# Kernel optimization log

Hardware: AMD Instinct MI355X
Metric: run time of the kernel (lower is better)

The kernel has to match this reference:

```python
import jax, jax.numpy as jnp
import numpy as np

N, S, D_MODEL, H = 8, 1024, 1024, 16
D = D_MODEL // H
NEG = -1e9


def setup_inputs() -> dict:
    key = jax.random.key(0)
    ks = jax.random.split(key, 12)
    s = 0.02
    q = jax.random.normal(ks[0], (N, S, D_MODEL), jnp.float32)
    k = jax.random.normal(ks[1], (N, S, D_MODEL), jnp.float32)
    v = jax.random.normal(ks[2], (N, S, D_MODEL), jnp.float32)
    # causal mask: 1 where masked (strict upper triangle)
    causal_mask = jnp.triu(jnp.ones((S, S), jnp.int32), k=1)
    # padding mask: 1 where key position is padding
    padding_mask = jax.random.randint(ks[3], (N, S), 0, 2, jnp.int32)
    Wq = jax.random.normal(ks[4], (D_MODEL, D_MODEL), jnp.float32) * s
    bq = jnp.zeros((D_MODEL,), jnp.float32)
    Wk = jax.random.normal(ks[5], (D_MODEL, D_MODEL), jnp.float32) * s
    bk = jnp.zeros((D_MODEL,), jnp.float32)
    Wv = jax.random.normal(ks[6], (D_MODEL, D_MODEL), jnp.float32) * s
    bv = jnp.zeros((D_MODEL,), jnp.float32)
    Wo = jax.random.normal(ks[7], (D_MODEL, D_MODEL), jnp.float32) * s
    bo = jnp.zeros((D_MODEL,), jnp.float32)
    return {"q": q, "k": k, "v": v, "causal_mask": causal_mask,
            "padding_mask": padding_mask, "Wq": Wq, "bq": bq, "Wk": Wk,
            "bk": bk, "Wv": Wv, "bv": bv, "Wo": Wo, "bo": bo}


def reference(q, k, v, causal_mask, padding_mask, Wq, bq, Wk, bk, Wv, bv, Wo, bo):
    n, qs, _ = q.shape
    # projections (nn.Linear: x @ W.T + b)
    qp = (q @ Wq.T + bq).reshape(n, qs, H, D).transpose(0, 2, 1, 3)  # [N,H,qS,D]
    kp = (k @ Wk.T + bk).reshape(n, -1, H, D).transpose(0, 2, 1, 3)  # [N,H,kS,D]
    vp = (v @ Wv.T + bv).reshape(n, -1, H, D).transpose(0, 2, 1, 3)  # [N,H,kS,D]
    # NOTE: faithful to source -- scale by sqrt(d_model), not sqrt(d_head)
    score = jnp.einsum('bhqd,bhkd->bhqk', qp, kp) / jnp.sqrt(jnp.float32(D_MODEL))
    score = jnp.where(causal_mask[None, None, :, :] == 1, NEG, score)
    score = jnp.where(padding_mask[:, None, None, :] == 1, NEG, score)
    w = jax.nn.softmax(score, axis=-1)  # dropout is identity in eval mode
    x = jnp.einsum('bhqk,bhkd->bhqd', w, vp)  # [N,H,qS,D]
    x = x.transpose(0, 2, 1, 3).reshape(n, qs, D_MODEL)
    x = x @ Wo.T + bo
    return (x, w)
```

## Files before the change

kernel.cpp:

```cpp
#include <hip/hip_runtime.h>

typedef __bf16 bf16;
typedef bf16 bf16x8 __attribute__((ext_vector_type(8)));
typedef bf16 bf16x4 __attribute__((ext_vector_type(4)));
typedef float f32x4 __attribute__((ext_vector_type(4)));

#define S_LEN 1024
#define DM    1024
#define NH    16
#define HD    64
#define NB    8
#define NEGV  (-1e9f)

#define EPI_HEADS 0
#define EPI_VT    1
#define EPI_OUT   2

__device__ __forceinline__ void async16(const bf16* g, const bf16* l) {
    __builtin_amdgcn_global_load_lds(
        (const __attribute__((address_space(1))) void*)g,
        (__attribute__((address_space(3))) void*)l, 16, 0, 0);
}

__global__ __launch_bounds__(256) void cast_all(
    const float* __restrict__ q, const float* __restrict__ k,
    const float* __restrict__ v, const float* __restrict__ wq,
    const float* __restrict__ wk, const float* __restrict__ wv,
    const float* __restrict__ wo, bf16* __restrict__ out)
{
    size_t idx = ((size_t)blockIdx.x * 256 + threadIdx.x) * 4;
    const float* src;
    size_t soff;
    if (idx < 25165824) {
        int seg = (int)(idx >> 23);
        soff = idx & 8388607;
        src = seg == 0 ? q : (seg == 1 ? k : v);
    } else {
        size_t r = idx - 25165824;
        int seg = (int)(r >> 20);
        soff = r & 1048575;
        src = seg == 0 ? wq : (seg == 1 ? wk : (seg == 2 ? wv : wo));
    }
    float4 val = *(const float4*)&src[soff];
    bf16x4 o = {(bf16)val.x, (bf16)val.y, (bf16)val.z, (bf16)val.w};
    *(bf16x4*)&out[idx] = o;
}

template<int EPI>
__global__ __launch_bounds__(256) void gemm_nt(
    const bf16* __restrict__ Ap, const bf16* __restrict__ Bp,
    const float* __restrict__ bias, void* __restrict__ Cp)
{
    __shared__ bf16 As[128][32];
    __shared__ bf16 Bs[128][32];

    const int tid    = threadIdx.x;
    const int l      = tid & 63;
    const int wid    = tid >> 6;
    const int wr     = wid >> 1, wc = wid & 1;
    const int lane15 = l & 15, quad = l >> 4;
    const int row0   = blockIdx.x * 128;
    const int col0   = blockIdx.y * 128;

    f32x4 acc[4][4];
    #pragma unroll
    for (int i = 0; i < 4; ++i)
        #pragma unroll
        for (int j = 0; j < 4; ++j)
            acc[i][j] = (f32x4){0.f, 0.f, 0.f, 0.f};

    for (int k0 = 0; k0 < 1024; k0 += 32) {
        #pragma unroll
        for (int j = 0; j < 2; ++j) {
            int cbase = j * 256 + wid * 64;
            int c = cbase + l;
            int r = c >> 2, kc = (c & 3) << 3;
            async16(&Ap[(size_t)(row0 + r) * 1024 + k0 + kc], &As[0][0] + cbase * 8);
            async16(&Bp[(size_t)(col0 + r) * 1024 + k0 + kc], &Bs[0][0] + cbase * 8);
        }
        __syncthreads();

        bf16x8 afr[4], bfr[4];
        #pragma unroll
        for (int tm = 0; tm < 4; ++tm)
            afr[tm] = *(const bf16x8*)&As[wr * 64 + tm * 16 + lane15][quad * 8];
        #pragma unroll
        for (int tn = 0; tn < 4; ++tn)
            bfr[tn] = *(const bf16x8*)&Bs[wc * 64 + tn * 16 + lane15][quad * 8];
        #pragma unroll
        for (int tm = 0; tm < 4; ++tm)
            #pragma unroll
            for (int tn = 0; tn < 4; ++tn)
                acc[tm][tn] = __builtin_amdgcn_mfma_f32_16x16x32_bf16(
                    afr[tm], bfr[tn], acc[tm][tn], 0, 0, 0);
        __syncthreads();
    }

    #pragma unroll
    for (int tm = 0; tm < 4; ++tm) {
        #pragma unroll
        for (int tn = 0; tn < 4; ++tn) {
            #pragma unroll
            for (int i = 0; i < 4; ++i) {
                int gr = row0 + wr * 64 + tm * 16 + quad * 4 + i;
                int gc = col0 + wc * 64 + tn * 16 + lane15;
                float vout = acc[tm][tn][i] + bias[gc];
                if constexpr (EPI == EPI_HEADS) {
                    int n = gr >> 10, s = gr & 1023, h = gc >> 6, d = gc & 63;
                    ((bf16*)Cp)[(((size_t)(n * NH + h) * S_LEN + s) << 6) + d] = (bf16)vout;
                } else if constexpr (EPI == EPI_VT) {
                    int n = gr >> 10, s = gr & 1023, h = gc >> 6, d = gc & 63;
                    ((bf16*)Cp)[(((size_t)(n * NH + h) * HD + d) << 10) + s] = (bf16)vout;
                } else {
                    ((float*)Cp)[(size_t)gr * DM + gc] = vout;
                }
            }
        }
    }
}

__global__ __launch_bounds__(256, 4) void attn_fused(
    const bf16* __restrict__ Qp, const bf16* __restrict__ Kp,
    const bf16* __restrict__ VpT, const int* __restrict__ pad,
    float* __restrict__ Wout, bf16* __restrict__ ctx)
{
    const int qblk = blockIdx.x;
    const int h = blockIdx.y, n = blockIdx.z;
    const int bh = n * NH + h;
    const bf16* Qb = Qp + (size_t)bh * S_LEN * HD;
    const bf16* Kb = Kp + (size_t)bh * S_LEN * HD;
    const bf16* Vb = VpT + (size_t)bh * HD * S_LEN;
    float* Wb = Wout + (size_t)bh * S_LEN * S_LEN;

    const int tid = threadIdx.x;
    const int l = tid & 63, wid = tid >> 6;
    const int lane15 = l & 15, quad = l >> 4;
    const int q0 = qblk * 16;
    const int q = q0 + lane15;
    const int qmax = q0 + 15;

    __shared__ bf16  P[16][1032];
    __shared__ float redM[4][16];
    __shared__ float redS[4][16];

    bf16x8 qf0 = *(const bf16x8*)&Qb[(size_t)q * HD + quad * 8];
    bf16x8 qf1 = *(const bf16x8*)&Qb[(size_t)q * HD + 32 + quad * 8];

    const int keyw = wid * 256;
    f32x4 sc[16];
    float mm = NEGV;

    #pragma unroll
    for (int t = 0; t < 16; ++t) {
        int kb = keyw + t * 16;
        if (kb <= qmax) {
            bf16x8 kf0 = *(const bf16x8*)&Kb[(size_t)(kb + lane15) * HD + quad * 8];
            bf16x8 kf1 = *(const bf16x8*)&Kb[(size_t)(kb + lane15) * HD + 32 + quad * 8];
            f32x4 a = (f32x4){0.f, 0.f, 0.f, 0.f};
            a = __builtin_amdgcn_mfma_f32_16x16x32_bf16(kf0, qf0, a, 0, 0, 0);
            a = __builtin_amdgcn_mfma_f32_16x16x32_bf16(kf1, qf1, a, 0, 0, 0);
            int4 pd = *(const int4*)&pad[n * S_LEN + kb + quad * 4];
            const int* pdi = (const int*)&pd;
            int key0 = kb + quad * 4;
            #pragma unroll
            for (int i = 0; i < 4; ++i) {
                float v = a[i] * 0.03125f;
                a[i] = (key0 + i > q || pdi[i] != 0) ? NEGV : v;
            }
            sc[t] = a;
            mm = fmaxf(mm, fmaxf(fmaxf(a[0], a[1]), fmaxf(a[2], a[3])));
        }
    }

    mm = fmaxf(mm, __shfl_xor(mm, 16));
    mm = fmaxf(mm, __shfl_xor(mm, 32));
    if (l < 16) redM[wid][l] = mm;
    __syncthreads();
    float m = fmaxf(fmaxf(redM[0][lane15], redM[1][lane15]),
                    fmaxf(redM[2][lane15], redM[3][lane15]));

    float vskip = __expf(NEGV - m);

    float sm = 0.f;
    #pragma unroll
    for (int t = 0; t < 16; ++t) {
        int kb = keyw + t * 16;
        if (kb <= qmax) {
            #pragma unroll
            for (int i = 0; i < 4; ++i) {
                float p = __expf(sc[t][i] - m);
                sc[t][i] = p;
                sm += p;
            }
        } else {
            sm += 4.f * vskip;
        }
    }
    sm += __shfl_xor(sm, 16);
    sm += __shfl_xor(sm, 32);
    if (l < 16) redS[wid][l] = sm;
    __syncthreads();
    float inv = 1.f / (redS[0][lane15] + redS[1][lane15] +
                       redS[2][lane15] + redS[3][lane15]);
    float wskip = vskip * inv;
    bool anyDeg = __ballot(m == NEGV) != 0;

    #pragma unroll
    for (int t = 0; t < 16; ++t) {
        int kb = keyw + t * 16;
        int off = kb + quad * 4;
        if (kb <= qmax) {
            float4 wv = {sc[t][0] * inv, sc[t][1] * inv,
                         sc[t][2] * inv, sc[t][3] * inv};
            *(float4*)&Wb[(size_t)q * S_LEN + off] = wv;
            bf16x4 pb = {(bf16)wv.x, (bf16)wv.y, (bf16)wv.z, (bf16)wv.w};
            *(bf16x4*)&P[lane15][off] = pb;
        } else {
            float4 wv = {wskip, wskip, wskip, wskip};
            *(float4*)&Wb[(size_t)q * S_LEN + off] = wv;
            bf16 pv = (bf16)wskip;
            bf16x4 pb = {pv, pv, pv, pv};
            *(bf16x4*)&P[lane15][off] = pb;
        }
    }
    __syncthreads();

    const int dbase = wid * 16;
    const int cEnd = anyDeg ? 32 : ((qmax >> 5) + 1);
    f32x4 o = (f32x4){0.f, 0.f, 0.f, 0.f};
    #pragma unroll 4
    for (int c = 0; c < cEnd; ++c) {
        bf16x8 a = *(const bf16x8*)&P[lane15][c * 32 + quad * 8];
        bf16x8 b = *(const bf16x8*)&Vb[(size_t)(dbase + lane15) * S_LEN + c * 32 + quad * 8];
        o = __builtin_amdgcn_mfma_f32_16x16x32_bf16(a, b, o, 0, 0, 0);
    }
    #pragma unroll
    for (int i = 0; i < 4; ++i) {
        int row = q0 + quad * 4 + i;
        ctx[((size_t)(n * S_LEN + row) << 10) + h * HD + dbase + lane15] = (bf16)o[i];
    }
}

extern "C" void kernel_launch(void* const* d_in, const int* in_sizes, int n_in,
                              void* d_out, int out_size, void* d_ws, size_t ws_size,
                              hipStream_t stream)
{
    const float* q   = (const float*)d_in[0];
    const float* k   = (const float*)d_in[1];
    const float* v   = (const float*)d_in[2];
    const int*   pad = (const int*)  d_in[4];
    const float* Wq  = (const float*)d_in[5];
    const float* bq  = (const float*)d_in[6];
    const float* Wk  = (const float*)d_in[7];
    const float* bk  = (const float*)d_in[8];
    const float* Wv  = (const float*)d_in[9];
    const float* bv  = (const float*)d_in[10];
    const float* Wo  = (const float*)d_in[11];
    const float* bo  = (const float*)d_in[12];

    float* x_out = (float*)d_out;
    float* w_out = x_out + (size_t)NB * S_LEN * DM;

    bf16* wsb = (bf16*)d_ws;
    bf16* Qc  = wsb;
    bf16* Wqb = wsb + 25165824;
    bf16* Wkb = wsb + 26214400;
    bf16* Wvb = wsb + 27262976;
    bf16* Wob = wsb + 28311552;
    bf16* Qp  = wsb + 29360128;
    bf16* Kp  = wsb + 37748736;
    bf16* VpT = wsb + 46137344;
    bf16* ctx = wsb + 54525952;
    bf16* Kc  = Qc + 8388608;
    bf16* Vc  = Qc + 16777216;

    cast_all<<<28672, 256, 0, stream>>>(q, k, v, Wq, Wk, Wv, Wo, wsb);

    gemm_nt<EPI_HEADS><<<dim3(64, 8), 256, 0, stream>>>(Qc, Wqb, bq, Qp);
    gemm_nt<EPI_HEADS><<<dim3(64, 8), 256, 0, stream>>>(Kc, Wkb, bk, Kp);
    gemm_nt<EPI_VT>   <<<dim3(64, 8), 256, 0, stream>>>(Vc, Wvb, bv, VpT);

    attn_fused<<<dim3(64, NH, NB), 256, 0, stream>>>(Qp, Kp, VpT, pad, w_out, ctx);

    gemm_nt<EPI_OUT><<<dim3(64, 8), 256, 0, stream>>>(ctx, Wob, bo, x_out);
}
```

Measured before the change: 962.6 us.

## Fuse QKV projections into one GEMM launch and remap attention blocks per XCD

Merges the three separate Q/K/V projection GEMMs into a single launch with 24 column blocks, where each block picks its input segment, weights and output layout. The 1/32 score scale is folded into the Q projection epilogue instead of being applied in attention. The attention grid is flattened to 1D and each block id is remapped so that all 64 query blocks of one (batch, head) land on the same XCD. The aim is better L2 reuse of K/V, fewer launches and a larger grid for the GEMM. The one added risk is that Q is now rounded to bf16 after scaling.

```diff
diff --git a/kernel.cpp b/kernel.cpp
--- a/kernel.cpp
+++ b/kernel.cpp
@@ -11,6 +11,7 @@
 #define HD    64
 #define NB    8
 #define NEGV  (-1e9f)
+#define QSCALE 0.03125f
 
 #define EPI_HEADS 0
 #define EPI_VT    1
@@ -41,9 +42,87 @@
         soff = r & 1048575;
         src = seg == 0 ? wq : (seg == 1 ? wk : (seg == 2 ? wv : wo));
     }
-    float4 val = *(const float4*)&src[soff];
+    f32x4 val = *(const f32x4*)&src[soff];
     bf16x4 o = {(bf16)val.x, (bf16)val.y, (bf16)val.z, (bf16)val.w};
     *(bf16x4*)&out[idx] = o;
+}
+
+__global__ __launch_bounds__(256) void gemm_qkv(
+    const bf16* __restrict__ Ap, const bf16* __restrict__ Ball,
+    const float* __restrict__ bq, const float* __restrict__ bk,
+    const float* __restrict__ bv, bf16* __restrict__ Qp,
+    bf16* __restrict__ Kp, bf16* __restrict__ VpT)
+{
+    __shared__ bf16 As[128][32];
+    __shared__ bf16 Bs[128][32];
+
+    const int tid    = threadIdx.x;
+    const int l      = tid & 63;
+    const int wid    = tid >> 6;
+    const int wr     = wid >> 1, wc = wid & 1;
+    const int lane15 = l & 15, quad = l >> 4;
+    const int row0   = blockIdx.x * 128;
+    const int seg    = blockIdx.y >> 3;
+    const int col0   = (blockIdx.y & 7) * 128;
+    const int brow0  = seg * 1024 + col0;
+
+    const bf16* Aseg = Ap + (size_t)seg * 8388608;
+    const float* bias = seg == 0 ? bq : (seg == 1 ? bk : bv);
+
+    f32x4 acc[4][4];
+    #pragma unroll
+    for (int i = 0; i < 4; ++i)
+        #pragma unroll
+        for (int j = 0; j < 4; ++j)
+            acc[i][j] = (f32x4){0.f, 0.f, 0.f, 0.f};
+
+    for (int k0 = 0; k0 < 1024; k0 += 32) {
+        #pragma unroll
+        for (int j = 0; j < 2; ++j) {
+            int cbase = j * 256 + wid * 64;
+            int c = cbase + l;
+            int r = c >> 2, kc = (c & 3) << 3;
+            async16(&Aseg[(size_t)(row0 + r) * 1024 + k0 + kc], &As[0][0] + cbase * 8);
+            async16(&Ball[(size_t)(brow0 + r) * 1024 + k0 + kc], &Bs[0][0] + cbase * 8);
+        }
+        __syncthreads();
+
+        bf16x8 afr[4], bfr[4];
+        #pragma unroll
+        for (int tm = 0; tm < 4; ++tm)
+            afr[tm] = *(const bf16x8*)&As[wr * 64 + tm * 16 + lane15][quad * 8];
+        #pragma unroll
+        for (int tn = 0; tn < 4; ++tn)
+            bfr[tn] = *(const bf16x8*)&Bs[wc * 64 + tn * 16 + lane15][quad * 8];
+        #pragma unroll
+        for (int tm = 0; tm < 4; ++tm)
+            #pragma unroll
+            for (int tn = 0; tn < 4; ++tn)
+                acc[tm][tn] = __builtin_amdgcn_mfma_f32_16x16x32_bf16(
+                    afr[tm], bfr[tn], acc[tm][tn], 0, 0, 0);
+        __syncthreads();
+    }
+
+    #pragma unroll
+    for (int tm = 0; tm < 4; ++tm) {
+        #pragma unroll
+        for (int tn = 0; tn < 4; ++tn) {
+            #pragma unroll
+            for (int i = 0; i < 4; ++i) {
+                int gr = row0 + wr * 64 + tm * 16 + quad * 4 + i;
+                int gc = col0 + wc * 64 + tn * 16 + lane15;
+                float vout = acc[tm][tn][i] + bias[gc];
+                int n = gr >> 10, s = gr & 1023, h = gc >> 6, d = gc & 63;
+                if (seg == 0) {
+                    Qp[(((size_t)(n * NH + h) * S_LEN + s) << 6) + d] = (bf16)(vout * QSCALE);
+                } else if (seg == 1) {
+                    Kp[(((size_t)(n * NH + h) * S_LEN + s) << 6) + d] = (bf16)vout;
+                } else {
+                    VpT[(((size_t)(n * NH + h) * HD + d) << 10) + s] = (bf16)vout;
+                }
+            }
+        }
+    }
 }
 
 template<int EPI>
@@ -124,9 +203,13 @@
     const bf16* __restrict__ VpT, const int* __restrict__ pad,
     float* __restrict__ Wout, bf16* __restrict__ ctx)
 {
-    const int qblk = blockIdx.x;
-    const int h = blockIdx.y, n = blockIdx.z;
-    const int bh = n * NH + h;
+    const int gid   = blockIdx.x;
+    const int xcd   = gid & 7;
+    const int t_    = gid >> 3;
+    const int qblk  = t_ & 63;
+    const int bh    = ((t_ >> 6) << 3) | xcd;
+    const int h = bh & 15, n = bh >> 4;
+
     const bf16* Qb = Qp + (size_t)bh * S_LEN * HD;
     const bf16* Kb = Kp + (size_t)bh * S_LEN * HD;
     const bf16* Vb = VpT + (size_t)bh * HD * S_LEN;
@@ -163,10 +246,8 @@
             const int* pdi = (const int*)&pd;
             int key0 = kb + quad * 4;
             #pragma unroll
-            for (int i = 0; i < 4; ++i) {
-                float v = a[i] * 0.03125f;
-                a[i] = (key0 + i > q || pdi[i] != 0) ? NEGV : v;
-            }
+            for (int i = 0; i < 4; ++i)
+                a[i] = (key0 + i > q || pdi[i] != 0) ? NEGV : a[i];
             sc[t] = a;
             mm = fmaxf(mm, fmaxf(fmaxf(a[0], a[1]), fmaxf(a[2], a[3])));
         }
@@ -210,14 +291,14 @@
         int kb = keyw + t * 16;
         int off = kb + quad * 4;
         if (kb <= qmax) {
-            float4 wv = {sc[t][0] * inv, sc[t][1] * inv,
-                         sc[t][2] * inv, sc[t][3] * inv};
-            *(float4*)&Wb[(size_t)q * S_LEN + off] = wv;
+            f32x4 wv = {sc[t][0] * inv, sc[t][1] * inv,
+                        sc[t][2] * inv, sc[t][3] * inv};
+            *(f32x4*)&Wb[(size_t)q * S_LEN + off] = wv;
             bf16x4 pb = {(bf16)wv.x, (bf16)wv.y, (bf16)wv.z, (bf16)wv.w};
             *(bf16x4*)&P[lane15][off] = pb;
         } else {
-            float4 wv = {wskip, wskip, wskip, wskip};
-            *(float4*)&Wb[(size_t)q * S_LEN + off] = wv;
+            f32x4 wv = {wskip, wskip, wskip, wskip};
+            *(f32x4*)&Wb[(size_t)q * S_LEN + off] = wv;
             bf16 pv = (bf16)wskip;
             bf16x4 pb = {pv, pv, pv, pv};
             *(bf16x4*)&P[lane15][off] = pb;
@@ -264,23 +345,17 @@
     bf16* wsb = (bf16*)d_ws;
     bf16* Qc  = wsb;
     bf16* Wqb = wsb + 25165824;
-    bf16* Wkb = wsb + 26214400;
-    bf16* Wvb = wsb + 27262976;
     bf16* Wob = wsb + 28311552;
     bf16* Qp  = wsb + 29360128;
     bf16* Kp  = wsb + 37748736;
     bf16* VpT = wsb + 46137344;
     bf16* ctx = wsb + 54525952;
-    bf16* Kc  = Qc + 8388608;
-    bf16* Vc  = Qc + 16777216;
 
     cast_all<<<28672, 256, 0, stream>>>(q, k, v, Wq, Wk, Wv, Wo, wsb);
 
-    gemm_nt<EPI_HEADS><<<dim3(64, 8), 256, 0, stream>>>(Qc, Wqb, bq, Qp);
-    gemm_nt<EPI_HEADS><<<dim3(64, 8), 256, 0, stream>>>(Kc, Wkb, bk, Kp);
-    gemm_nt<EPI_VT>   <<<dim3(64, 8), 256, 0, stream>>>(Vc, Wvb, bv, VpT);
-
-    attn_fused<<<dim3(64, NH, NB), 256, 0, stream>>>(Qp, Kp, VpT, pad, w_out, ctx);
+    gemm_qkv<<<dim3(64, 24), 256, 0, stream>>>(Qc, Wqb, bq, bk, bv, Qp, Kp, VpT);
+
+    attn_fused<<<dim3(8192), 256, 0, stream>>>(Qp, Kp, VpT, pad, w_out, ctx);
 
     gemm_nt<EPI_OUT><<<dim3(64, 8), 256, 0, stream>>>(ctx, Wob, bo, x_out);
 }
```

Measured after the change: 930.9 us. 3.3% less time.
